# Kernel tuning notes

Hardware: AMD Instinct MI355X
Metric: run time of the kernel (lower is better)

The kernel has to match this reference:

```python
import jax, jax.numpy as jnp
import numpy as np

D_MODEL = 1024
NUM_HEADS = 16
D_K = D_MODEL // NUM_HEADS
D_MLP = 4096
EPS = 1e-5


def setup_inputs() -> dict:
    key = jax.random.key(0)
    ks = jax.random.split(key, 16)
    s = 0.02
    inp = {
        "x": jax.random.normal(ks[0], (2, 2048, D_MODEL), dtype=jnp.float32),
        "Wq": jax.random.normal(ks[1], (D_MODEL, D_MODEL), dtype=jnp.float32) * s,
        "bq": jnp.zeros((D_MODEL,), jnp.float32),
        "Wk": jax.random.normal(ks[2], (D_MODEL, D_MODEL), dtype=jnp.float32) * s,
        "bk": jnp.zeros((D_MODEL,), jnp.float32),
        "Wv": jax.random.normal(ks[3], (D_MODEL, D_MODEL), dtype=jnp.float32) * s,
        "bv": jnp.zeros((D_MODEL,), jnp.float32),
        "Wo": jax.random.normal(ks[4], (D_MODEL, D_MODEL), dtype=jnp.float32) * s,
        "bo": jnp.zeros((D_MODEL,), jnp.float32),
        "W1": jax.random.normal(ks[5], (D_MODEL, D_MLP), dtype=jnp.float32) * s,
        "b1": jnp.zeros((D_MLP,), jnp.float32),
        "W2": jax.random.normal(ks[6], (D_MLP, D_MODEL), dtype=jnp.float32) * s,
        "b2": jnp.zeros((D_MODEL,), jnp.float32),
        "ln1_g": jnp.ones((D_MODEL,), jnp.float32),
        "ln1_b": jnp.zeros((D_MODEL,), jnp.float32),
        "ln2_g": jnp.ones((D_MODEL,), jnp.float32),
        "ln2_b": jnp.zeros((D_MODEL,), jnp.float32),
    }
    return inp


def _layer_norm(x, g, b):
    mu = jnp.mean(x, axis=-1, keepdims=True)
    var = jnp.var(x, axis=-1, keepdims=True)
    return (x - mu) * jax.lax.rsqrt(var + EPS) * g + b


def _split_heads(x):
    b, s, _ = x.shape
    return x.reshape(b, s, NUM_HEADS, D_K).transpose(0, 2, 1, 3)  # [b,h,s,dk]


def reference(x, Wq, bq, Wk, bk, Wv, bv, Wo, bo, W1, b1, W2, b2,
              ln1_g, ln1_b, ln2_g, ln2_b):
    b, s, _ = x.shape
    q = _split_heads(x @ Wq + bq)
    k = _split_heads(x @ Wk + bk)
    v = _split_heads(x @ Wv + bv)
    # [b,h,s,s] scores, scaled by sqrt(d_k) as in the original
    score = jnp.einsum("bhqd,bhkd->bhqk", q, k) / jnp.sqrt(jnp.float32(D_K))
    attn = jax.nn.softmax(score, axis=-1)
    out = jnp.einsum("bhqk,bhkd->bhqd", attn, v)
    out = out.transpose(0, 2, 1, 3).reshape(b, s, D_MODEL)
    out = out @ Wo + bo
    # residual + norm1 (dropout is identity in eval)
    x = _layer_norm(x + out, ln1_g, ln1_b)
    # feed-forward
    h = jax.nn.relu(x @ W1 + b1)
    ff = h @ W2 + b2
    x = _layer_norm(x + ff, ln2_g, ln2_b)
    return x
```

## Files before the change

### kernel.cpp

```cpp
#include <hip/hip_runtime.h>
#include <hip/hip_bf16.h>
#include <cstdint>

#define DEV __device__ __forceinline__

typedef __attribute__((ext_vector_type(8))) __bf16 bf16x8;
typedef __attribute__((ext_vector_type(4))) float f32x4;

DEV uint16_t f2b(float f) {
  __hip_bfloat16 h = __float2bfloat16(f);
  return *(uint16_t*)&h;
}
DEV uint32_t pkbf2(float a, float b) {
  return (uint32_t)f2b(a) | ((uint32_t)f2b(b) << 16);
}

DEV void gload_lds16(const void* g, void* l) {
  __builtin_amdgcn_global_load_lds(
      (const __attribute__((address_space(1))) void*)g,
      (__attribute__((address_space(3))) void*)l, 16, 0, 0);
}

DEV bf16x8 scale8(bf16x8 v, float sc) {
  union { bf16x8 b; uint16_t u[8]; } in, out;
  in.b = v;
#pragma unroll
  for (int i = 0; i < 8; i++) {
    float x = __uint_as_float(((uint32_t)in.u[i]) << 16);
    out.u[i] = f2b(x * sc);
  }
  return out.b;
}

__global__ __launch_bounds__(256) void cast_bf16_kernel(
    const float* __restrict__ src, uint16_t* __restrict__ dst, int n4) {
  int i = blockIdx.x * 256 + threadIdx.x;
  if (i < n4) {
    float4 v = ((const float4*)src)[i];
    uint2 r;
    r.x = pkbf2(v.x, v.y);
    r.y = pkbf2(v.z, v.w);
    ((uint2*)dst)[i] = r;
  }
}

__global__ __launch_bounds__(256) void transpose_w(
    const float* __restrict__ src, uint16_t* __restrict__ dst, int R, int C) {
  __shared__ float t[32][33];
  int c0 = blockIdx.x * 32, r0 = blockIdx.y * 32;
  int tx = threadIdx.x & 31, ty = threadIdx.x >> 5;
#pragma unroll
  for (int i = 0; i < 4; i++)
    t[ty + 8 * i][tx] = src[(size_t)(r0 + ty + 8 * i) * C + c0 + tx];
  __syncthreads();
#pragma unroll
  for (int i = 0; i < 4; i++)
    dst[(size_t)(c0 + ty + 8 * i) * R + r0 + tx] = f2b(t[tx][ty + 8 * i]);
}

__global__ __launch_bounds__(256) void transpose_w3(
    const float* __restrict__ s0, const float* __restrict__ s1,
    const float* __restrict__ s2, uint16_t* __restrict__ dst) {
  __shared__ float t[32][33];
  const float* src = blockIdx.z == 0 ? s0 : (blockIdx.z == 1 ? s1 : s2);
  uint16_t* d = dst + (size_t)blockIdx.z * 1024 * 1024;
  int c0 = blockIdx.x * 32, r0 = blockIdx.y * 32;
  int tx = threadIdx.x & 31, ty = threadIdx.x >> 5;
#pragma unroll
  for (int i = 0; i < 4; i++)
    t[ty + 8 * i][tx] = src[(size_t)(r0 + ty + 8 * i) * 1024 + c0 + tx];
  __syncthreads();
#pragma unroll
  for (int i = 0; i < 4; i++)
    d[(size_t)(c0 + ty + 8 * i) * 1024 + r0 + tx] = f2b(t[tx][ty + 8 * i]);
}

__global__ __launch_bounds__(256) void transpose_v(
    const uint16_t* __restrict__ qkv, uint16_t* __restrict__ Vt) {
  __shared__ uint16_t t[32][33];
  int bh = blockIdx.z, b = bh >> 4, h = bh & 15;
  int s0 = blockIdx.x * 32, d0 = blockIdx.y * 32;
  int tx = threadIdx.x & 31, ty = threadIdx.x >> 5;
#pragma unroll
  for (int i = 0; i < 4; i++)
    t[ty + 8 * i][tx] =
        qkv[(size_t)(b * 2048 + s0 + ty + 8 * i) * 3072 + 2048 + h * 64 + d0 + tx];
  __syncthreads();
#pragma unroll
  for (int i = 0; i < 4; i++)
    Vt[((size_t)bh * 64 + d0 + ty + 8 * i) * 2048 + s0 + tx] = t[tx][ty + 8 * i];
}

__global__ __launch_bounds__(256) void concat3(
    const float* __restrict__ a, const float* __restrict__ b,
    const float* __restrict__ c, float* __restrict__ o) {
  int i = blockIdx.x * 256 + threadIdx.x;
  o[i] = i < 1024 ? a[i] : (i < 2048 ? b[i - 1024] : c[i - 2048]);
}

template <int MODE, int NSPLIT, int BK>
__global__ __launch_bounds__(256) void gemm_bt(
    const uint16_t* __restrict__ A, const uint16_t* __restrict__ Bt,
    const float* __restrict__ bias, void* __restrict__ Cv, void* __restrict__ Cv2,
    int M, int N, int K, int nx) {
  __shared__ uint16_t As[2][128 * BK];
  __shared__ uint16_t Bs[2][128 * BK];
  int nwg = gridDim.x, bid = blockIdx.x;
  int cpx = nwg >> 3;
  int swzb = (bid & 7) * cpx + (bid >> 3);
  int ntile = nwg / NSPLIT;
  int sp = swzb / ntile, r = swzb % ntile;
  int n0 = (r % nx) * 128, m0 = (r / nx) * 128;
  int Klen = K / NSPLIT;
  int tid = threadIdx.x, w = tid >> 6, l = tid & 63;
  int wr = w >> 1, wc = w & 1;
  int lr = l & 15, lg = l >> 4, lk8 = lg * 8;
  f32x4 acc[4][4] = {};
  const uint16_t* Ab = A + (size_t)m0 * K + sp * Klen;
  const uint16_t* Bb = Bt + (size_t)n0 * K + sp * Klen;

  auto stage = [&](int buf, int k0) {
    if (BK == 32) {
#pragma unroll
      for (int i = 0; i < 2; i++) {
        int c = 2 * w + i;
        int rr = c * 16 + (l >> 2);
        gload_lds16(Ab + (size_t)rr * K + k0 + (l & 3) * 8, &As[buf][c * 512]);
        gload_lds16(Bb + (size_t)rr * K + k0 + (l & 3) * 8, &Bs[buf][c * 512]);
      }
    } else {
      int colb = (((l & 7) ^ ((l >> 3) & 7)) << 4);
#pragma unroll
      for (int i = 0; i < 4; i++) {
        int c = 4 * w + i;
        int rr = c * 8 + (l >> 3);
        gload_lds16((const uint8_t*)(Ab + (size_t)rr * K + k0) + colb,
                    &As[buf][c * 512]);
        gload_lds16((const uint8_t*)(Bb + (size_t)rr * K + k0) + colb,
                    &Bs[buf][c * 512]);
      }
    }
  };

  stage(0, 0);
  __syncthreads();

  for (int k0 = 0; k0 < Klen; k0 += BK) {
    int cur = (k0 / BK) & 1;
    if (k0 + BK < Klen) stage(cur ^ 1, k0 + BK);
    if (BK == 32) {
      bf16x8 af[4], bf[4];
#pragma unroll
      for (int m = 0; m < 4; m++)
        af[m] = *(const bf16x8*)&As[cur][(wr * 64 + m * 16 + lr) * 32 + lk8];
#pragma unroll
      for (int n = 0; n < 4; n++)
        bf[n] = *(const bf16x8*)&Bs[cur][(wc * 64 + n * 16 + lr) * 32 + lk8];
#pragma unroll
      for (int m = 0; m < 4; m++)
#pragma unroll
        for (int n = 0; n < 4; n++)
          acc[m][n] = __builtin_amdgcn_mfma_f32_16x16x32_bf16(af[m], bf[n], acc[m][n], 0, 0, 0);
    } else {
      int sw = (lr & 7) << 4;
#pragma unroll
      for (int ks = 0; ks < 2; ks++) {
        int off = ((ks << 6) | (lg << 4)) ^ sw;
        bf16x8 af[4], bf[4];
#pragma unroll
        for (int m = 0; m < 4; m++)
          af[m] = *(const bf16x8*)((const uint8_t*)&As[cur][(wr * 64 + m * 16 + lr) * 64] + off);
#pragma unroll
        for (int n = 0; n < 4; n++)
          bf[n] = *(const bf16x8*)((const uint8_t*)&Bs[cur][(wc * 64 + n * 16 + lr) * 64] + off);
#pragma unroll
        for (int m = 0; m < 4; m++)
#pragma unroll
          for (int n = 0; n < 4; n++)
            acc[m][n] = __builtin_amdgcn_mfma_f32_16x16x32_bf16(af[m], bf[n], acc[m][n], 0, 0, 0);
      }
    }
    __syncthreads();
  }

  void* dstv = (NSPLIT == 1 || sp == 0) ? Cv : Cv2;
  int g4 = lg * 4;
#pragma unroll
  for (int m = 0; m < 4; m++) {
    int row = m0 + wr * 64 + m * 16 + g4;
#pragma unroll
    for (int n = 0; n < 4; n++) {
      int col = n0 + wc * 64 + n * 16 + lr;
      float bv = (NSPLIT == 1 || sp == 0) ? bias[col] : 0.f;
#pragma unroll
      for (int j = 0; j < 4; j++) {
        float v = acc[m][n][j] + bv;
        if (MODE == 2) v = fmaxf(v, 0.f);
        size_t idx = (size_t)(row + j) * N + col;
        if (MODE == 0) ((float*)dstv)[idx] = v;
        else           ((uint16_t*)dstv)[idx] = f2b(v);
      }
    }
  }
}

__global__ __launch_bounds__(256, 2) void attn_fused(
    const uint16_t* __restrict__ qkv, const uint16_t* __restrict__ Vt,
    uint16_t* __restrict__ outb) {
  constexpr int LQ = 3072;
  constexpr float SC = 0.18033688f;
  int L = blockIdx.x;
  int qb = (L >> 3) & 15;
  int bh = (L & 7) + 8 * (L >> 7);
  int b = bh >> 4, h = bh & 15;
  int w = threadIdx.x >> 6, l = threadIdx.x & 63;
  int lr = l & 15, lg = l >> 4;
  int qbase = qb * 128 + w * 32;

  __shared__ uint16_t Kbuf[2][2][64 * 64];
  __shared__ uint16_t Vbuf[2][2][64 * 64];
  __shared__ uint16_t Plds[4][2][16 * 64];
  uint16_t* PwA = &Plds[w][0][0];
  uint16_t* PwB = &Plds[w][1][0];

  const uint16_t* qrowA = qkv + (size_t)(b * 2048 + qbase + lr) * LQ + h * 64;
  const uint16_t* qrowB = qrowA + (size_t)16 * LQ;
  bf16x8 qA0 = scale8(*(const bf16x8*)(qrowA + lg * 8), SC);
  bf16x8 qA1 = scale8(*(const bf16x8*)(qrowA + 32 + lg * 8), SC);
  bf16x8 qB0 = scale8(*(const bf16x8*)(qrowB + lg * 8), SC);
  bf16x8 qB1 = scale8(*(const bf16x8*)(qrowB + 32 + lg * 8), SC);

  float rsA = 0.f, rsB = 0.f;
  f32x4 oA[4] = {}, oB[4] = {};

  const uint8_t* kq = (const uint8_t*)qkv;
  const uint8_t* vq = (const uint8_t*)Vt;
  int colb = (((l & 7) ^ ((l >> 3) & 7)) << 4);
  int Rl = w * 16 + (l >> 3);

  auto stageKV = [&](int buf, int kb) {
#pragma unroll
    for (int s2 = 0; s2 < 2; s2++) {
#pragma unroll
      for (int c2 = 0; c2 < 2; c2++) {
        int R = Rl + c2 * 8;
        const uint8_t* ks =
            kq + ((size_t)(b * 2048 + kb + s2 * 64 + R) * LQ + 1024 + h * 64) * 2 + colb;
        gload_lds16(ks, &Kbuf[buf][s2][(w * 16 + c2 * 8) * 64]);
        const uint8_t* vs =
            vq + ((size_t)(bh * 64 + R) * 2048 + kb + s2 * 64) * 2 + colb;
        gload_lds16(vs, &Vbuf[buf][s2][(w * 16 + c2 * 8) * 64]);
      }
    }
  };

  stageKV(0, 0);
  __syncthreads();

  int swz = (lr & 7) << 4;
  for (int kb = 0; kb < 2048; kb += 128) {
    int cur = (kb >> 7) & 1;
    if (kb + 128 < 2048) stageKV(cur ^ 1, kb + 128);

#pragma unroll
    for (int s2 = 0; s2 < 2; s2++) {
      const uint8_t* Kb = (const uint8_t*)Kbuf[cur][s2];
      const uint8_t* Vb = (const uint8_t*)Vbuf[cur][s2];
      f32x4 sA[4], sB[4];
      __builtin_amdgcn_s_setprio(1);
#pragma unroll
      for (int t = 0; t < 4; t++) {
        const uint8_t* rb = Kb + (16 * t + lr) * 128;
        bf16x8 k0 = *(const bf16x8*)(rb + ((lg << 4) ^ swz));
        bf16x8 k1 = *(const bf16x8*)(rb + ((64 | (lg << 4)) ^ swz));
        f32x4 zA = {};
        zA = __builtin_amdgcn_mfma_f32_16x16x32_bf16(k0, qA0, zA, 0, 0, 0);
        zA = __builtin_amdgcn_mfma_f32_16x16x32_bf16(k1, qA1, zA, 0, 0, 0);
        sA[t] = zA;
        f32x4 zB = {};
        zB = __builtin_amdgcn_mfma_f32_16x16x32_bf16(k0, qB0, zB, 0, 0, 0);
        zB = __builtin_amdgcn_mfma_f32_16x16x32_bf16(k1, qB1, zB, 0, 0, 0);
        sB[t] = zB;
      }
      __builtin_amdgcn_s_setprio(0);
#pragma unroll
      for (int t = 0; t < 4; t++) {
        float a0 = __builtin_amdgcn_exp2f(sA[t][0]);
        float a1 = __builtin_amdgcn_exp2f(sA[t][1]);
        float a2 = __builtin_amdgcn_exp2f(sA[t][2]);
        float a3 = __builtin_amdgcn_exp2f(sA[t][3]);
        rsA += (a0 + a1) + (a2 + a3);
        uint2 pa;
        pa.x = pkbf2(a0, a1);
        pa.y = pkbf2(a2, a3);
        *(uint2*)((uint8_t*)PwA + lr * 128 + ((t * 32 + lg * 8) ^ swz)) = pa;
        float b0 = __builtin_amdgcn_exp2f(sB[t][0]);
        float b1 = __builtin_amdgcn_exp2f(sB[t][1]);
        float b2 = __builtin_amdgcn_exp2f(sB[t][2]);
        float b3 = __builtin_amdgcn_exp2f(sB[t][3]);
        rsB += (b0 + b1) + (b2 + b3);
        uint2 pb;
        pb.x = pkbf2(b0, b1);
        pb.y = pkbf2(b2, b3);
        *(uint2*)((uint8_t*)PwB + lr * 128 + ((t * 32 + lg * 8) ^ swz)) = pb;
      }
      __builtin_amdgcn_wave_barrier();
      bf16x8 pA0 = *(const bf16x8*)((const uint8_t*)PwA + lr * 128 + ((lg << 4) ^ swz));
      bf16x8 pA1 = *(const bf16x8*)((const uint8_t*)PwA + lr * 128 + ((64 | (lg << 4)) ^ swz));
      bf16x8 pB0 = *(const bf16x8*)((const uint8_t*)PwB + lr * 128 + ((lg << 4) ^ swz));
      bf16x8 pB1 = *(const bf16x8*)((const uint8_t*)PwB + lr * 128 + ((64 | (lg << 4)) ^ swz));
      __builtin_amdgcn_s_setprio(1);
#pragma unroll
      for (int t = 0; t < 4; t++) {
        const uint8_t* rb = Vb + (16 * t + lr) * 128;
        bf16x8 v0 = *(const bf16x8*)(rb + ((lg << 4) ^ swz));
        bf16x8 v1 = *(const bf16x8*)(rb + ((64 | (lg << 4)) ^ swz));
        oA[t] = __builtin_amdgcn_mfma_f32_16x16x32_bf16(v0, pA0, oA[t], 0, 0, 0);
        oA[t] = __builtin_amdgcn_mfma_f32_16x16x32_bf16(v1, pA1, oA[t], 0, 0, 0);
        oB[t] = __builtin_amdgcn_mfma_f32_16x16x32_bf16(v0, pB0, oB[t], 0, 0, 0);
        oB[t] = __builtin_amdgcn_mfma_f32_16x16x32_bf16(v1, pB1, oB[t], 0, 0, 0);
      }
      __builtin_amdgcn_s_setprio(0);
      if (s2 == 0) __builtin_amdgcn_wave_barrier();
    }
    __syncthreads();
  }
  rsA += __shfl_xor(rsA, 16);
  rsA += __shfl_xor(rsA, 32);
  rsB += __shfl_xor(rsB, 16);
  rsB += __shfl_xor(rsB, 32);
  float invA = 1.f / rsA, invB = 1.f / rsB;
  uint16_t* orowA = outb + (size_t)(b * 2048 + qbase + lr) * 1024 + h * 64;
  uint16_t* orowB = orowA + (size_t)16 * 1024;
#pragma unroll
  for (int t = 0; t < 4; t++) {
    uint2 ra;
    ra.x = pkbf2(oA[t][0] * invA, oA[t][1] * invA);
    ra.y = pkbf2(oA[t][2] * invA, oA[t][3] * invA);
    *(uint2*)(orowA + t * 16 + lg * 4) = ra;
    uint2 rb2;
    rb2.x = pkbf2(oB[t][0] * invB, oB[t][1] * invB);
    rb2.y = pkbf2(oB[t][2] * invB, oB[t][3] * invB);
    *(uint2*)(orowB + t * 16 + lg * 4) = rb2;
  }
}

template <int XBF, int WF32, int WB16, int NR>
__global__ __launch_bounds__(256) void ln_res(
    const void* __restrict__ xr, const float* __restrict__ r0,
    const float* __restrict__ r1, const float* __restrict__ gam,
    const float* __restrict__ bet, float* __restrict__ of32,
    uint16_t* __restrict__ ob16) {
  int row = blockIdx.x, t = threadIdx.x;
  int w = t >> 6, l = t & 63;
  float v0, v1, v2, v3;
  if (XBF) {
    uint2 u = ((const uint2*)((const uint16_t*)xr + (size_t)row * 1024))[t];
    v0 = __uint_as_float((u.x & 0xffffu) << 16);
    v1 = __uint_as_float(u.x & 0xffff0000u);
    v2 = __uint_as_float((u.y & 0xffffu) << 16);
    v3 = __uint_as_float(u.y & 0xffff0000u);
  } else {
    float4 xv = ((const float4*)((const float*)xr + (size_t)row * 1024))[t];
    v0 = xv.x; v1 = xv.y; v2 = xv.z; v3 = xv.w;
  }
  float4 rv = ((const float4*)(r0 + (size_t)row * 1024))[t];
  v0 += rv.x; v1 += rv.y; v2 += rv.z; v3 += rv.w;
  if (NR == 2) {
    float4 r2 = ((const float4*)(r1 + (size_t)row * 1024))[t];
    v0 += r2.x; v1 += r2.y; v2 += r2.z; v3 += r2.w;
  }
  float s = v0 + v1 + v2 + v3;
  float sq = v0 * v0 + v1 * v1 + v2 * v2 + v3 * v3;
#pragma unroll
  for (int d = 1; d < 64; d <<= 1) {
    s += __shfl_xor(s, d);
    sq += __shfl_xor(sq, d);
  }
  __shared__ float red[8];
  if (l == 0) { red[w] = s; red[4 + w] = sq; }
  __syncthreads();
  s = red[0] + red[1] + red[2] + red[3];
  sq = red[4] + red[5] + red[6] + red[7];
  float mean = s * (1.f / 1024.f);
  float var = sq * (1.f / 1024.f) - mean * mean;
  float rstd = rsqrtf(var + 1e-5f);
  float4 gv = ((const float4*)gam)[t];
  float4 bv = ((const float4*)bet)[t];
  float y0 = (v0 - mean) * rstd * gv.x + bv.x;
  float y1 = (v1 - mean) * rstd * gv.y + bv.y;
  float y2 = (v2 - mean) * rstd * gv.z + bv.z;
  float y3 = (v3 - mean) * rstd * gv.w + bv.w;
  if (WF32) {
    float4 yv; yv.x = y0; yv.y = y1; yv.z = y2; yv.w = y3;
    ((float4*)(of32 + (size_t)row * 1024))[t] = yv;
  }
  if (WB16) {
    uint2 r;
    r.x = pkbf2(y0, y1);
    r.y = pkbf2(y2, y3);
    ((uint2*)(ob16 + (size_t)row * 1024))[t] = r;
  }
}

static constexpr size_t OFF_XB    = 0;
static constexpr size_t OFF_WQKVT = (size_t)8 << 20;
static constexpr size_t OFF_WOT   = (size_t)14 << 20;
static constexpr size_t OFF_W1T   = (size_t)16 << 20;
static constexpr size_t OFF_W2T   = (size_t)24 << 20;
static constexpr size_t OFF_BIAS  = (size_t)32 << 20;
static constexpr size_t OFF_QKV   = OFF_BIAS + ((size_t)64 << 10);
static constexpr size_t OFF_VT    = OFF_QKV + ((size_t)24 << 20);
static constexpr size_t OFF_PROJ  = OFF_VT + ((size_t)8 << 20);
static constexpr size_t OFF_LN1B  = OFF_PROJ + ((size_t)16 << 20);
static constexpr size_t OFF_PROJ2 = OFF_LN1B + ((size_t)8 << 20);

extern "C" void kernel_launch(void* const* d_in, const int* in_sizes, int n_in,
                              void* d_out, int out_size, void* d_ws, size_t ws_size,
                              hipStream_t stream) {
  const float* x   = (const float*)d_in[0];
  const float* Wq  = (const float*)d_in[1];
  const float* bq  = (const float*)d_in[2];
  const float* Wk  = (const float*)d_in[3];
  const float* bk  = (const float*)d_in[4];
  const float* Wv  = (const float*)d_in[5];
  const float* bv  = (const float*)d_in[6];
  const float* Wo  = (const float*)d_in[7];
  const float* bo  = (const float*)d_in[8];
  const float* W1  = (const float*)d_in[9];
  const float* b1  = (const float*)d_in[10];
  const float* W2  = (const float*)d_in[11];
  const float* b2  = (const float*)d_in[12];
  const float* g1  = (const float*)d_in[13];
  const float* be1 = (const float*)d_in[14];
  const float* g2  = (const float*)d_in[15];
  const float* be2 = (const float*)d_in[16];
  float* out = (float*)d_out;
  uint8_t* ws = (uint8_t*)d_ws;

  uint16_t* xb    = (uint16_t*)(ws + OFF_XB);
  uint16_t* wqkt  = (uint16_t*)(ws + OFF_WQKVT);
  uint16_t* wot   = (uint16_t*)(ws + OFF_WOT);
  uint16_t* w1t   = (uint16_t*)(ws + OFF_W1T);
  uint16_t* w2t   = (uint16_t*)(ws + OFF_W2T);
  float*    bqkv  = (float*)(ws + OFF_BIAS);
  uint16_t* qkvb  = (uint16_t*)(ws + OFF_QKV);
  uint16_t* vt    = (uint16_t*)(ws + OFF_VT);
  float*    proj  = (float*)(ws + OFF_PROJ);
  float*    proj2 = (float*)(ws + OFF_PROJ2);
  uint16_t* ln1b  = (uint16_t*)(ws + OFF_LN1B);
  uint16_t* attnb = (uint16_t*)(ws + OFF_XB);
  uint16_t* hbuf  = (uint16_t*)(ws + OFF_QKV);

  cast_bf16_kernel<<<4096, 256, 0, stream>>>(x, xb, 4096 * 1024 / 4);
  transpose_w3<<<dim3(32, 32, 3), 256, 0, stream>>>(Wq, Wk, Wv, wqkt);
  transpose_w<<<dim3(32, 32), 256, 0, stream>>>(Wo, wot, 1024, 1024);
  transpose_w<<<dim3(128, 32), 256, 0, stream>>>(W1, w1t, 1024, 4096);
  transpose_w<<<dim3(32, 128), 256, 0, stream>>>(W2, w2t, 4096, 1024);
  concat3<<<12, 256, 0, stream>>>(bq, bk, bv, bqkv);
  gemm_bt<1, 1, 32><<<768, 256, 0, stream>>>(xb, wqkt, bqkv, qkvb, nullptr,
                                             4096, 3072, 1024, 24);
  transpose_v<<<dim3(64, 2, 32), 256, 0, stream>>>(qkvb, vt);
  attn_fused<<<512, 256, 0, stream>>>(qkvb, vt, attnb);
  gemm_bt<0, 2, 64><<<512, 256, 0, stream>>>(attnb, wot, bo, proj, proj2,
                                             4096, 1024, 1024, 8);
  ln_res<0, 0, 1, 2><<<4096, 256, 0, stream>>>(x, proj, proj2, g1, be1,
                                               nullptr, ln1b);
  gemm_bt<2, 1, 64><<<1024, 256, 0, stream>>>(ln1b, w1t, b1, hbuf, nullptr,
                                              4096, 4096, 1024, 32);
  gemm_bt<0, 2, 64><<<512, 256, 0, stream>>>(hbuf, w2t, b2, proj, proj2,
                                             4096, 1024, 4096, 8);
  ln_res<1, 1, 0, 2><<<4096, 256, 0, stream>>>(ln1b, proj, proj2, g2, be2,
                                               out, nullptr);
}
```

Baseline: 228.6 us.

## Add 256x256-tile 8-wave GEMM with interleaved prefetch for FFN up-projection

Adds a new gemm256 kernel that uses 256x256 output tiles with 512 threads, double-buffered LDS with XOR-swizzled direct global-to-LDS loads, and next-tile staging interleaved across the MFMA phases with setprio. It replaces the 128-tile gemm_bt for the W1 GEMM (4096x4096x1024, ReLU, bf16 output). The larger tile raises arithmetic intensity and cuts global traffic per FLOP. In exchange it uses 128 KB of LDS and many accumulator registers, and launches only 256 workgroups, which may limit occupancy and CU coverage.

```diff
diff --git a/kernel.cpp b/kernel.cpp
--- a/kernel.cpp
+++ b/kernel.cpp
@@ -199,6 +199,107 @@
         size_t idx = (size_t)(row + j) * N + col;
         if (MODE == 0) ((float*)dstv)[idx] = v;
         else           ((uint16_t*)dstv)[idx] = f2b(v);
+      }
+    }
+  }
+}
+
+template <int MODE>
+__global__ __launch_bounds__(512, 2) void gemm256(
+    const uint16_t* __restrict__ A, const uint16_t* __restrict__ Bt,
+    const float* __restrict__ bias, void* __restrict__ Cv,
+    int M, int N, int K, int nx) {
+  __shared__ uint16_t As[2][256 * 64];
+  __shared__ uint16_t Bs[2][256 * 64];
+  int nwg = gridDim.x, bid = blockIdx.x;
+  int cpx = nwg >> 3;
+  int swzb = (bid & 7) * cpx + (bid >> 3);
+  int n0 = (swzb % nx) * 256, m0 = (swzb / nx) * 256;
+  int tid = threadIdx.x, w = tid >> 6, l = tid & 63;
+  int wr = w >> 2, wc = w & 3;
+  int lr = l & 15, lg = l >> 4;
+  f32x4 acc[8][4] = {};
+  const uint16_t* Ab = A + (size_t)m0 * K;
+  const uint16_t* Bb = Bt + (size_t)n0 * K;
+  int colb = (((l & 7) ^ (l >> 3)) << 4);
+  int srl = l >> 3;
+
+  auto stageH = [&](int buf, int k0, int h) {
+    const uint16_t* base = (h < 2) ? Ab : Bb;
+    uint16_t* lds = (h < 2) ? &As[buf][0] : &Bs[buf][0];
+    int hh = (h & 1) * 128;
+#pragma unroll
+    for (int j = 0; j < 2; j++) {
+      int rr = hh + j * 64 + w * 8;
+      gload_lds16((const uint8_t*)(base + (size_t)(rr + srl) * K + k0) + colb,
+                  &lds[rr * 64]);
+    }
+  };
+
+#pragma unroll
+  for (int h = 0; h < 4; h++) stageH(0, 0, h);
+  asm volatile("s_waitcnt vmcnt(0)" ::: "memory");
+  __builtin_amdgcn_s_barrier();
+
+  int nt = K >> 6;
+  int swr = (lr & 7) << 4;
+  for (int t = 0; t < nt; t++) {
+    int buf = t & 1;
+    bf16x8 bfr[2][4];
+#pragma unroll
+    for (int ks = 0; ks < 2; ks++) {
+#pragma unroll
+      for (int mq = 0; mq < 2; mq++) {
+        const int ph = ks * 2 + mq;
+        int off = ((ks << 6) | (lg << 4)) ^ swr;
+        bf16x8 af[4];
+#pragma unroll
+        for (int m = 0; m < 4; m++) {
+          int row = wr * 128 + (mq * 4 + m) * 16 + lr;
+          af[m] = *(const bf16x8*)((const uint8_t*)&As[buf][row * 64] + off);
+        }
+        if (mq == 0) {
+#pragma unroll
+          for (int n = 0; n < 4; n++) {
+            int row = wc * 64 + n * 16 + lr;
+            bfr[ks][n] = *(const bf16x8*)((const uint8_t*)&Bs[buf][row * 64] + off);
+          }
+        }
+        if (t + 1 < nt) {
+          if (ph == 0) { stageH(buf ^ 1, (t + 1) * 64, 0); stageH(buf ^ 1, (t + 1) * 64, 1); }
+          if (ph == 1) { stageH(buf ^ 1, (t + 1) * 64, 2); stageH(buf ^ 1, (t + 1) * 64, 3); }
+        }
+        __builtin_amdgcn_s_barrier();
+        asm volatile("s_waitcnt lgkmcnt(0)" ::: "memory");
+        __builtin_amdgcn_sched_barrier(0);
+        __builtin_amdgcn_s_setprio(1);
+#pragma unroll
+        for (int m = 0; m < 4; m++)
+#pragma unroll
+          for (int n = 0; n < 4; n++)
+            acc[mq * 4 + m][n] = __builtin_amdgcn_mfma_f32_16x16x32_bf16(
+                af[m], bfr[ks][n], acc[mq * 4 + m][n], 0, 0, 0);
+        __builtin_amdgcn_s_setprio(0);
+        if (ph == 3) asm volatile("s_waitcnt vmcnt(0)" ::: "memory");
+        __builtin_amdgcn_s_barrier();
+      }
+    }
+  }
+
+#pragma unroll
+  for (int m = 0; m < 8; m++) {
+    int row = m0 + wr * 128 + m * 16 + lg * 4;
+#pragma unroll
+    for (int n = 0; n < 4; n++) {
+      int col = n0 + wc * 64 + n * 16 + lr;
+      float bv = bias[col];
+#pragma unroll
+      for (int j = 0; j < 4; j++) {
+        float v = acc[m][n][j] + bv;
+        if (MODE == 2) v = fmaxf(v, 0.f);
+        size_t idx = (size_t)(row + j) * N + col;
+        if (MODE == 0) ((float*)Cv)[idx] = v;
+        else           ((uint16_t*)Cv)[idx] = f2b(v);
       }
     }
   }
@@ -466,8 +567,7 @@
                                              4096, 1024, 1024, 8);
   ln_res<0, 0, 1, 2><<<4096, 256, 0, stream>>>(x, proj, proj2, g1, be1,
                                                nullptr, ln1b);
-  gemm_bt<2, 1, 64><<<1024, 256, 0, stream>>>(ln1b, w1t, b1, hbuf, nullptr,
-                                              4096, 4096, 1024, 32);
+  gemm256<2><<<256, 512, 0, stream>>>(ln1b, w1t, b1, hbuf, 4096, 4096, 1024, 16);
   gemm_bt<0, 2, 64><<<512, 256, 0, stream>>>(hbuf, w2t, b2, proj, proj2,
                                              4096, 1024, 4096, 8);
   ln_res<1, 1, 0, 2><<<4096, 256, 0, stream>>>(ln1b, proj, proj2, g2, be2,
```

Result: faster. 221.6 us (-3.0%).
